# Kernel tuning notes

Measured on AMD Instinct MI355X. Metric: run time of the kernel, lower is better.

Reference implementation:

```python
import jax, jax.numpy as jnp
import numpy as np

N, E, D, H = 50000, 600000, 128, 128
SLOPE = 0.01  # default negative_slope of F.leaky_relu / nn.LeakyReLU


def leaky(x):
    return jnp.where(x >= 0, x, SLOPE * x)


def gcn_conv(x, src, dst, W, b, n):
    """PyG GCNConv: x' = D^{-1/2}(A+I)D^{-1/2} (x W) + b, symmetric norm with self-loops."""
    h = x @ W  # [n, out]
    ones = jnp.ones(src.shape[0], h.dtype)
    deg = jax.ops.segment_sum(ones, dst, num_segments=n) + 1.0  # +1 for self-loop
    dinv = jax.lax.rsqrt(deg)  # deg >= 1 always
    norm = dinv[src] * dinv[dst]  # per-edge coefficient
    msg = h[src] * norm[:, None]  # gather + scale: [E, out]
    agg = jax.ops.segment_sum(msg, dst, num_segments=n)  # scatter-add
    agg = agg + h * (dinv * dinv)[:, None]  # self-loop term
    return agg + b


def setup_inputs() -> dict:
    key = jax.random.key(0)
    ks = jax.random.split(key, 16)
    kaiming = lambda k, fi, fo: jax.random.normal(k, (fi, fo), jnp.float32) * np.sqrt(2.0 / fi)
    return {
        "x": jax.random.normal(ks[0], (N, D), jnp.float32),
        "edge_index": jax.random.randint(ks[1], (2, E), 0, N, jnp.int64 if jax.config.jax_enable_x64 else jnp.int32),
        "gen_data": jax.random.normal(ks[2], (N, H), jnp.float32),
        "Wc1": kaiming(ks[3], D, H), "bc1": jnp.zeros((H,), jnp.float32),
        "Wc2": kaiming(ks[4], H, H), "bc2": jnp.zeros((H,), jnp.float32),
        "Wm1": kaiming(ks[5], H, H), "bm1": jnp.zeros((H,), jnp.float32),
        "Wm2": kaiming(ks[6], H, H), "bm2": jnp.zeros((H,), jnp.float32),
        "Wp1": kaiming(ks[7], H, H), "bp1": jnp.zeros((H,), jnp.float32),
        "Wp2": kaiming(ks[8], H, H), "bp2": jnp.zeros((H,), jnp.float32),
    }


def reference(x, edge_index, gen_data, Wc1, bc1, Wc2, bc2, Wm1, bm1, Wm2, bm2, Wp1, bp1, Wp2, bp2):
    src, dst = edge_index[0], edge_index[1]
    lambd = 0.5
    # GraphEncoder4Link
    h = leaky(gcn_conv(x, src, dst, Wc1, bc1, N))
    h = leaky(gcn_conv(h, src, dst, Wc2, bc2, N) + h)
    h = leaky((leaky(h @ Wm1 + bm1) @ Wm2 + bm2) + h)
    # lambd interpolation with gen_data
    out = lambd * h + (1.0 - lambd) * gen_data
    # proj MLP
    out = leaky(leaky(out @ Wp1 + bp1) @ Wp2 + bp2)
    return out
```

## Files before the change

kernel.cpp:

```cpp
#include <hip/hip_runtime.h>
#include <cstdint>
#include <cstddef>

#define HH 128
#define SLOPE 0.01f

typedef __attribute__((ext_vector_type(8))) __bf16 bf16x8;
typedef __attribute__((ext_vector_type(8))) unsigned short ushort8v;
typedef __attribute__((ext_vector_type(4))) float f32x4;

__device__ __forceinline__ float lrelu(float x) { return x >= 0.f ? x : SLOPE * x; }
__device__ __forceinline__ unsigned short f2b(float f) {
  union { float f; unsigned u; } v; v.f = f;
  unsigned r = v.u + 0x7fffu + ((v.u >> 16) & 1u);
  return (unsigned short)(r >> 16);
}
__device__ __forceinline__ float b2f(unsigned short u) {
  union { unsigned u; float f; } v; v.u = ((unsigned)u) << 16; return v.f;
}

__device__ __forceinline__ int lofs(int r, int k) {
  return (r << 7) + ((((k >> 3) ^ r) & 15) << 3) + (k & 7);
}

#define WAVE_SYNC() asm volatile("s_waitcnt lgkmcnt(0)" ::: "memory")

__device__ __forceinline__ void gll16(const void* g, void* l) {
  __builtin_amdgcn_global_load_lds((const __attribute__((address_space(1))) void*)g,
                                   (__attribute__((address_space(3))) void*)l, 16, 0, 0);
}


__global__ __launch_bounds__(256) void count_kernel(const int* __restrict__ dst,
                                                    int* __restrict__ cnt,
                                                    int* __restrict__ rank, int nE) {
  int e = blockIdx.x * 256 + threadIdx.x;
  if (e < nE) rank[e] = atomicAdd(&cnt[dst[e]], 1);
}

__global__ __launch_bounds__(1024) void scan1_kernel(int* __restrict__ cnt,
                                                     int* __restrict__ rowptr,
                                                     int* __restrict__ bsum,
                                                     float* __restrict__ dinv, int n) {
  __shared__ int wsum[16];
  const int tid = threadIdx.x;
  const int lane = tid & 63, wid = tid >> 6;
  int i = blockIdx.x * 1024 + tid;
  int v = (i < n) ? cnt[i] : 0;
  int vp = (v + 7) & ~7;
  int x = vp;
#pragma unroll
  for (int off = 1; off < 64; off <<= 1) {
    int y = __shfl_up(x, off, 64);
    if (lane >= off) x += y;
  }
  if (lane == 63) wsum[wid] = x;
  __syncthreads();
  if (tid == 0) {
    int s = 0;
#pragma unroll
    for (int w = 0; w < 16; ++w) { int t = wsum[w]; wsum[w] = s; s += t; }
    bsum[blockIdx.x] = s;
  }
  __syncthreads();
  if (i < n) {
    rowptr[i] = wsum[wid] + x - vp;
    dinv[i] = rsqrtf((float)v + 1.0f);
  }
}

__global__ __launch_bounds__(64) void scan2_kernel(int* __restrict__ bsum, int nb,
                                                   int* __restrict__ rowptr, int n) {
  int lane = threadIdx.x;
  int v = (lane < nb) ? bsum[lane] : 0;
  int x = v;
#pragma unroll
  for (int off = 1; off < 64; off <<= 1) {
    int y = __shfl_up(x, off, 64);
    if (lane >= off) x += y;
  }
  int tot = __shfl(x, nb - 1);
  if (lane < nb) bsum[lane] = x - v;
  if (lane == 0) rowptr[n] = tot;
}

__global__ __launch_bounds__(1024) void scan3_kernel(int* __restrict__ rowptr,
                                                     const int* __restrict__ bsum, int n) {
  int i = blockIdx.x * 1024 + threadIdx.x;
  if (i < n) rowptr[i] += bsum[blockIdx.x];
}

__global__ __launch_bounds__(256) void fill_kernel(const int* __restrict__ src,
                                                   const int* __restrict__ dst,
                                                   const int* __restrict__ rowptr,
                                                   const int* __restrict__ rank,
                                                   const float* __restrict__ dinv,
                                                   int2* __restrict__ csr, int nE) {
  int e = blockIdx.x * 256 + threadIdx.x;
  if (e >= nE) return;
  int d = dst[e], s = src[e];
  int pos = rowptr[d] + rank[e];
  int2 ent;
  ent.x = s;
  ent.y = __float_as_int(dinv[s] * dinv[d]);
  csr[pos] = ent;
}

__global__ __launch_bounds__(256) void pack_kernel(const float* W0, const float* W1,
                                                   const float* W2, const float* W3,
                                                   const float* W4, const float* W5,
                                                   unsigned short* __restrict__ out) {
  const float* Ws[6] = {W0, W1, W2, W3, W4, W5};
  const float* W = Ws[blockIdx.y];
  int f = blockIdx.x * 256 + threadIdx.x;
  int j = f & 7, L = (f >> 3) & 63, c = (f >> 9) & 7, t = f >> 12;
  int k = t * 32 + (L >> 4) * 8 + j;
  int n = c * 16 + (L & 15);
  out[(size_t)blockIdx.y * 16384 + f] = f2b(W[k * HH + n]);
}


__device__ __forceinline__ void mfma_ldsW(const bf16x8 af[4],
                                          const unsigned short* __restrict__ Wl,
                                          int lane, f32x4 acc[8]) {
#pragma unroll
  for (int c = 0; c < 8; ++c) acc[c] = (f32x4){0.f, 0.f, 0.f, 0.f};
#pragma unroll
  for (int t = 0; t < 4; ++t) {
    bf16x8 wf[8];
#pragma unroll
    for (int c = 0; c < 8; ++c) wf[c] = *(const bf16x8*)&Wl[(t * 8 + c) * 512 + lane * 8];
#pragma unroll
    for (int c = 0; c < 8; ++c)
      acc[c] = __builtin_amdgcn_mfma_f32_16x16x32_bf16(af[t], wf[c], acc[c], 0, 0, 0);
  }
}

__device__ __forceinline__ void lds_afrags16(const unsigned short* __restrict__ Tl,
                                             int m, int quad, bf16x8 af[4]) {
#pragma unroll
  for (int t = 0; t < 4; ++t)
    af[t] = *(const bf16x8*)&Tl[lofs(m, t * 32 + quad * 8)];
}


__global__ __launch_bounds__(256, 1) void gemm_conv(const float* __restrict__ A,
                                                    const unsigned short* __restrict__ Wp,
                                                    unsigned short* __restrict__ out, int nrows) {
  __shared__ __align__(16) unsigned short Wl[16384];
  const int tid = threadIdx.x;
  const int lane = tid & 63, wave = tid >> 6;
  const int row0 = blockIdx.x * 64 + wave * 16;
  const int m = lane & 15, quad = lane >> 4;

#pragma unroll
  for (int i = 0; i < 8; ++i)
    gll16((const uint4*)Wp + i * 256 + tid, (uint4*)Wl + i * 256 + wave * 64);

  const int gr = row0 + m;
  const bool rok = gr < nrows;
  const float* Arow = A + (size_t)gr * HH;
  bf16x8 af[4];
#pragma unroll
  for (int t = 0; t < 4; ++t) {
    const int k = t * 32 + quad * 8;
    float4 lo = make_float4(0.f, 0.f, 0.f, 0.f), hi = lo;
    if (rok) {
      lo = *(const float4*)(Arow + k);
      hi = *(const float4*)(Arow + k + 4);
    }
    union { ushort8v u; bf16x8 b; } cv;
    cv.u[0] = f2b(lo.x); cv.u[1] = f2b(lo.y); cv.u[2] = f2b(lo.z); cv.u[3] = f2b(lo.w);
    cv.u[4] = f2b(hi.x); cv.u[5] = f2b(hi.y); cv.u[6] = f2b(hi.z); cv.u[7] = f2b(hi.w);
    af[t] = cv.b;
  }

  __syncthreads();

  f32x4 acc[8];
  mfma_ldsW(af, Wl, lane, acc);

#pragma unroll
  for (int c = 0; c < 8; ++c) {
    int col = c * 16 + m;
#pragma unroll
    for (int g = 0; g < 4; ++g) {
      int row = row0 + quad * 4 + g;
      if (row < nrows) out[(size_t)row * HH + col] = f2b(acc[c][g]);
    }
  }
}


template <int RES, int OUTBF>
__global__ __launch_bounds__(256) void agg_kernel(const unsigned short* __restrict__ h,
                                                  const int* __restrict__ rowptr,
                                                  const int2* __restrict__ csr,
                                                  const float* __restrict__ dinv,
                                                  const float* __restrict__ bias,
                                                  const float* __restrict__ res,
                                                  void* __restrict__ outv, int n) {
  int node = blockIdx.x * 4 + (threadIdx.x >> 6);
  if (node >= n) return;
  const int lane = threadIdx.x & 63;
  const int p = lane >> 5;
  const int c4 = (lane & 31) << 2;
  int j = rowptr[node];
  const int end = rowptr[node + 1];

  const float di = dinv[node];
  const ushort4 hs = *(const ushort4*)(h + (size_t)node * HH + c4);
  const float4 b = *(const float4*)(bias + c4);
  float4 rr = make_float4(0.f, 0.f, 0.f, 0.f);
  if (RES) rr = *(const float4*)(res + (size_t)node * HH + c4);

  float a0 = 0.f, a1 = 0.f, a2 = 0.f, a3 = 0.f;
  for (; j < end; j += 8) {
    int2 e[4];
    ushort4 r[4];
#pragma unroll
    for (int q = 0; q < 4; ++q) e[q] = csr[j + 2 * q + p];
#pragma unroll
    for (int q = 0; q < 4; ++q) r[q] = *(const ushort4*)(h + (size_t)e[q].x * HH + c4);
#pragma unroll
    for (int q = 0; q < 4; ++q) {
      float nv = __int_as_float(e[q].y);
      a0 = fmaf(b2f(r[q].x), nv, a0); a1 = fmaf(b2f(r[q].y), nv, a1);
      a2 = fmaf(b2f(r[q].z), nv, a2); a3 = fmaf(b2f(r[q].w), nv, a3);
    }
  }

  a0 += __shfl_xor(a0, 32);
  a1 += __shfl_xor(a1, 32);
  a2 += __shfl_xor(a2, 32);
  a3 += __shfl_xor(a3, 32);

  if (p == 0) {
    const float d2 = di * di;
    float o0 = a0 + b2f(hs.x) * d2 + b.x + rr.x;
    float o1 = a1 + b2f(hs.y) * d2 + b.y + rr.y;
    float o2 = a2 + b2f(hs.z) * d2 + b.z + rr.z;
    float o3 = a3 + b2f(hs.w) * d2 + b.w + rr.w;
    o0 = lrelu(o0); o1 = lrelu(o1); o2 = lrelu(o2); o3 = lrelu(o3);
    if (OUTBF) {
      ushort4 o;
      o.x = f2b(o0); o.y = f2b(o1); o.z = f2b(o2); o.w = f2b(o3);
      *(ushort4*)((unsigned short*)outv + (size_t)node * HH + c4) = o;
    } else {
      *(float4*)((float*)outv + (size_t)node * HH + c4) = make_float4(o0, o1, o2, o3);
    }
  }
}


__global__ __launch_bounds__(256, 1) void fusedMLP(const unsigned short* __restrict__ f2bf,
                                                   const unsigned short* __restrict__ Wm1p,
                                                   const unsigned short* __restrict__ Wm2p,
                                                   const unsigned short* __restrict__ Wp1p,
                                                   const unsigned short* __restrict__ Wp2p,
                                                   const float* __restrict__ bm1,
                                                   const float* __restrict__ bm2,
                                                   const float* __restrict__ bp1,
                                                   const float* __restrict__ bp2,
                                                   const float* __restrict__ gen,
                                                   float* __restrict__ out, int n) {
  __shared__ __align__(16) unsigned short Wl[2][16384];
  __shared__ __align__(16) unsigned short Tl[4][16 * HH];
  const int tid = threadIdx.x;
  const int lane = tid & 63, wave = tid >> 6;
  const int row0 = blockIdx.x * 64 + wave * 16;
  const int m = lane & 15, quad = lane >> 4;
  unsigned short* T = Tl[wave];

#pragma unroll
  for (int i = 0; i < 8; ++i) {
    gll16((const uint4*)Wm1p + i * 256 + tid, (uint4*)Wl[0] + i * 256 + wave * 64);
    gll16((const uint4*)Wm2p + i * 256 + tid, (uint4*)Wl[1] + i * 256 + wave * 64);
  }

#pragma unroll
  for (int i = 0; i < 4; ++i) {
    int idx = i * 64 + lane;
    int r = idx >> 4, k = (idx & 15) << 3;
    int gr = row0 + r;
    ushort8v v = {0, 0, 0, 0, 0, 0, 0, 0};
    if (gr < n) v = *(const ushort8v*)(f2bf + (size_t)gr * HH + k);
    *(ushort8v*)&T[lofs(r, k)] = v;
  }

  ushort4 genb[8];
#pragma unroll
  for (int i = 0; i < 8; ++i) {
    int idx = i * 64 + lane;
    int r = idx >> 5, c4 = (idx & 31) << 2;
    int gr = row0 + r;
    float4 v = make_float4(0.f, 0.f, 0.f, 0.f);
    if (gr < n) v = *(const float4*)(gen + (size_t)gr * HH + c4);
    genb[i].x = f2b(v.x); genb[i].y = f2b(v.y); genb[i].z = f2b(v.z); genb[i].w = f2b(v.w);
  }

  float bvAll[4][8];
#pragma unroll
  for (int cc = 0; cc < 8; ++cc) {
    int col = cc * 16 + m;
    bvAll[0][cc] = bm1[col];
    bvAll[1][cc] = bm2[col];
    bvAll[2][cc] = bp1[col];
    bvAll[3][cc] = bp2[col];
  }

  __syncthreads();

  bf16x8 af[4];
  f32x4 acc[8];

  lds_afrags16(T, m, quad, af);
  unsigned f2res[8][2];
#pragma unroll
  for (int cc = 0; cc < 8; ++cc) {
    int col = cc * 16 + m;
#pragma unroll
    for (int gp = 0; gp < 2; ++gp) {
      int lr = quad * 4 + gp * 2;
      f2res[cc][gp] = (unsigned)T[lofs(lr, col)] | ((unsigned)T[lofs(lr + 1, col)] << 16);
    }
  }
  mfma_ldsW(af, Wl[0], lane, acc);
  WAVE_SYNC();
#pragma unroll
  for (int cc = 0; cc < 8; ++cc) {
    int col = cc * 16 + m;
#pragma unroll
    for (int g = 0; g < 4; ++g)
      T[lofs(quad * 4 + g, col)] = f2b(lrelu(acc[cc][g] + bvAll[0][cc]));
  }
  __syncthreads();

#pragma unroll
  for (int i = 0; i < 8; ++i)
    gll16((const uint4*)Wp1p + i * 256 + tid, (uint4*)Wl[0] + i * 256 + wave * 64);

  lds_afrags16(T, m, quad, af);
  WAVE_SYNC();
#pragma unroll
  for (int i = 0; i < 8; ++i) {
    int idx = i * 64 + lane;
    int r = idx >> 5, c4 = (idx & 31) << 2;
    *(ushort4*)&T[lofs(r, c4)] = genb[i];
  }
  mfma_ldsW(af, Wl[1], lane, acc);
  WAVE_SYNC();
#pragma unroll
  for (int cc = 0; cc < 8; ++cc) {
    int col = cc * 16 + m;
#pragma unroll
    for (int g = 0; g < 4; ++g) {
      int lr = quad * 4 + g;
      unsigned fr = f2res[cc][g >> 1];
      float f2v = b2f((unsigned short)((g & 1) ? (fr >> 16) : (fr & 0xffffu)));
      float v = lrelu(acc[cc][g] + bvAll[1][cc] + f2v);
      float gv = b2f(T[lofs(lr, col)]);
      T[lofs(lr, col)] = f2b(0.5f * (v + gv));
    }
  }
  __syncthreads();

#pragma unroll
  for (int i = 0; i < 8; ++i)
    gll16((const uint4*)Wp2p + i * 256 + tid, (uint4*)Wl[1] + i * 256 + wave * 64);

  lds_afrags16(T, m, quad, af);
  mfma_ldsW(af, Wl[0], lane, acc);
  WAVE_SYNC();
#pragma unroll
  for (int cc = 0; cc < 8; ++cc) {
    int col = cc * 16 + m;
#pragma unroll
    for (int g = 0; g < 4; ++g)
      T[lofs(quad * 4 + g, col)] = f2b(lrelu(acc[cc][g] + bvAll[2][cc]));
  }
  __syncthreads();

  lds_afrags16(T, m, quad, af);
  mfma_ldsW(af, Wl[1], lane, acc);
#pragma unroll
  for (int cc = 0; cc < 8; ++cc) {
    int col = cc * 16 + m;
#pragma unroll
    for (int g = 0; g < 4; ++g) {
      int row = row0 + quad * 4 + g;
      if (row < n) out[(size_t)row * HH + col] = lrelu(acc[cc][g] + bvAll[3][cc]);
    }
  }
}


extern "C" void kernel_launch(void* const* d_in, const int* in_sizes, int n_in,
                              void* d_out, int out_size, void* d_ws, size_t ws_size,
                              hipStream_t stream) {
  const float* x   = (const float*)d_in[0];
  const int* ei    = (const int*)d_in[1];
  const float* gen = (const float*)d_in[2];
  const float* Wc1 = (const float*)d_in[3];
  const float* bc1 = (const float*)d_in[4];
  const float* Wc2 = (const float*)d_in[5];
  const float* bc2 = (const float*)d_in[6];
  const float* Wm1 = (const float*)d_in[7];
  const float* bm1 = (const float*)d_in[8];
  const float* Wm2 = (const float*)d_in[9];
  const float* bm2 = (const float*)d_in[10];
  const float* Wp1 = (const float*)d_in[11];
  const float* bp1 = (const float*)d_in[12];
  const float* Wp2 = (const float*)d_in[13];
  const float* bp2 = (const float*)d_in[14];

  const int N = in_sizes[0] / HH;
  const int E = in_sizes[1] / 2;
  const int* src = ei;
  const int* dst = ei + E;

  const size_t Epad = (size_t)E + 8 * (size_t)N;

  char* ws = (char*)d_ws;
  size_t off = 0;
  auto alloc = [&](size_t bytes) { void* p = ws + off; off += (bytes + 255) & ~(size_t)255; return p; };
  float* dinv            = (float*)alloc((size_t)N * 4);
  int*   rowptr          = (int*)  alloc((size_t)(N + 1) * 4);
  int*   cnt             = (int*)  alloc((size_t)N * 4);
  int*   bsum            = (int*)  alloc((size_t)64 * 4);
  int*   rank            = (int*)  alloc((size_t)E * 4);
  int2*  csr             = (int2*) alloc(Epad * 8);
  unsigned short* h_bf   = (unsigned short*)alloc((size_t)N * HH * 2);
  unsigned short* t2_bf  = (unsigned short*)alloc((size_t)N * HH * 2);
  unsigned short* f2_bf  = (unsigned short*)alloc((size_t)N * HH * 2);
  float* f1_f32          = (float*)alloc((size_t)N * HH * 4);
  unsigned short* packed = (unsigned short*)alloc((size_t)6 * 16384 * 2);
  float* fOut = (float*)d_out;

  const int cblocks = (N + 63) / 64;
  const int eblocks = (E + 255) / 256;
  const int ablocks = (N + 3) / 4;
  const int sblocks = (N + 1023) / 1024;

  pack_kernel<<<dim3(64, 6), 256, 0, stream>>>(Wc1, Wc2, Wm1, Wm2, Wp1, Wp2, packed);

  hipMemsetAsync(cnt, 0, (size_t)N * 4, stream);
  hipMemsetAsync(csr, 0, Epad * 8, stream);
  count_kernel<<<eblocks, 256, 0, stream>>>(dst, cnt, rank, E);
  scan1_kernel<<<sblocks, 1024, 0, stream>>>(cnt, rowptr, bsum, dinv, N);
  scan2_kernel<<<1, 64, 0, stream>>>(bsum, sblocks, rowptr, N);
  scan3_kernel<<<sblocks, 1024, 0, stream>>>(rowptr, bsum, N);
  fill_kernel<<<eblocks, 256, 0, stream>>>(src, dst, rowptr, rank, dinv, csr, E);

  gemm_conv<<<cblocks, 256, 0, stream>>>(x, packed + 0 * 16384, h_bf, N);
  agg_kernel<0, 0><<<ablocks, 256, 0, stream>>>(h_bf, rowptr, csr, dinv, bc1, nullptr, f1_f32, N);
  gemm_conv<<<cblocks, 256, 0, stream>>>(f1_f32, packed + 1 * 16384, t2_bf, N);
  agg_kernel<1, 1><<<ablocks, 256, 0, stream>>>(t2_bf, rowptr, csr, dinv, bc2, f1_f32, f2_bf, N);
  fusedMLP<<<cblocks, 256, 0, stream>>>(f2_bf,
                                        packed + 2 * 16384, packed + 3 * 16384,
                                        packed + 4 * 16384, packed + 5 * 16384,
                                        bm1, bm2, bp1, bp2, gen, fOut, N);
}
```

Before: 280.8 us.

## Merge preprocessing launches: pack+count, scan2 into scan3, fill into first GEMM

Combines the weight pack and edge-count kernels into one launch, folds the single-block scan of block sums into each scan3 block, and runs CSR fill blocks alongside the first GEMM in one grid. The two memsets become one by making cnt and csr contiguous in the workspace. This cuts kernel launches and the serial gaps between small kernels. The trade-offs are redundant per-block scan work and fill blocks that now run under the GEMM's launch bounds and LDS allocation.

```diff
diff --git a/kernel.cpp b/kernel.cpp
--- a/kernel.cpp
+++ b/kernel.cpp
@@ -31,12 +31,30 @@
 }
 
 
-__global__ __launch_bounds__(256) void count_kernel(const int* __restrict__ dst,
+__global__ __launch_bounds__(256) void k_pack_count(const float* W0, const float* W1,
+                                                    const float* W2, const float* W3,
+                                                    const float* W4, const float* W5,
+                                                    unsigned short* __restrict__ outp,
+                                                    const int* __restrict__ dst,
                                                     int* __restrict__ cnt,
                                                     int* __restrict__ rank, int nE) {
-  int e = blockIdx.x * 256 + threadIdx.x;
-  if (e < nE) rank[e] = atomicAdd(&cnt[dst[e]], 1);
-}
+  const int bb = blockIdx.x;
+  const int tid = threadIdx.x;
+  if (bb < 384) {
+    const float* Ws[6] = {W0, W1, W2, W3, W4, W5};
+    const int mat = bb >> 6;
+    const float* W = Ws[mat];
+    int f = (bb & 63) * 256 + tid;
+    int j = f & 7, L = (f >> 3) & 63, c = (f >> 9) & 7, t = f >> 12;
+    int k = t * 32 + (L >> 4) * 8 + j;
+    int n = c * 16 + (L & 15);
+    outp[(size_t)mat * 16384 + f] = f2b(W[k * HH + n]);
+  } else {
+    int e = (bb - 384) * 256 + tid;
+    if (e < nE) rank[e] = atomicAdd(&cnt[dst[e]], 1);
+  }
+}
+
 
 __global__ __launch_bounds__(1024) void scan1_kernel(int* __restrict__ cnt,
                                                      int* __restrict__ rowptr,
@@ -69,54 +87,26 @@
   }
 }
 
-__global__ __launch_bounds__(64) void scan2_kernel(int* __restrict__ bsum, int nb,
-                                                   int* __restrict__ rowptr, int n) {
-  int lane = threadIdx.x;
-  int v = (lane < nb) ? bsum[lane] : 0;
-  int x = v;
-#pragma unroll
-  for (int off = 1; off < 64; off <<= 1) {
-    int y = __shfl_up(x, off, 64);
-    if (lane >= off) x += y;
-  }
-  int tot = __shfl(x, nb - 1);
-  if (lane < nb) bsum[lane] = x - v;
-  if (lane == 0) rowptr[n] = tot;
-}
-
 __global__ __launch_bounds__(1024) void scan3_kernel(int* __restrict__ rowptr,
-                                                     const int* __restrict__ bsum, int n) {
-  int i = blockIdx.x * 1024 + threadIdx.x;
-  if (i < n) rowptr[i] += bsum[blockIdx.x];
-}
-
-__global__ __launch_bounds__(256) void fill_kernel(const int* __restrict__ src,
-                                                   const int* __restrict__ dst,
-                                                   const int* __restrict__ rowptr,
-                                                   const int* __restrict__ rank,
-                                                   const float* __restrict__ dinv,
-                                                   int2* __restrict__ csr, int nE) {
-  int e = blockIdx.x * 256 + threadIdx.x;
-  if (e >= nE) return;
-  int d = dst[e], s = src[e];
-  int pos = rowptr[d] + rank[e];
-  int2 ent;
-  ent.x = s;
-  ent.y = __float_as_int(dinv[s] * dinv[d]);
-  csr[pos] = ent;
-}
-
-__global__ __launch_bounds__(256) void pack_kernel(const float* W0, const float* W1,
-                                                   const float* W2, const float* W3,
-                                                   const float* W4, const float* W5,
-                                                   unsigned short* __restrict__ out) {
-  const float* Ws[6] = {W0, W1, W2, W3, W4, W5};
-  const float* W = Ws[blockIdx.y];
-  int f = blockIdx.x * 256 + threadIdx.x;
-  int j = f & 7, L = (f >> 3) & 63, c = (f >> 9) & 7, t = f >> 12;
-  int k = t * 32 + (L >> 4) * 8 + j;
-  int n = c * 16 + (L & 15);
-  out[(size_t)blockIdx.y * 16384 + f] = f2b(W[k * HH + n]);
+                                                     const int* __restrict__ bsum,
+                                                     int n, int nb) {
+  __shared__ int spfx, stot;
+  const int tid = threadIdx.x;
+  if (tid < 64) {
+    int v = (tid < nb) ? bsum[tid] : 0;
+    int x = v;
+#pragma unroll
+    for (int off = 1; off < 64; off <<= 1) {
+      int y = __shfl_up(x, off, 64);
+      if (tid >= off) x += y;
+    }
+    if (tid == (int)blockIdx.x) spfx = x - v;
+    if (tid == nb - 1) stot = x;
+  }
+  __syncthreads();
+  int i = blockIdx.x * 1024 + tid;
+  if (i < n) rowptr[i] += spfx;
+  if (blockIdx.x == 0 && tid == 0) rowptr[n] = stot;
 }
 
 
@@ -143,14 +133,14 @@
     af[t] = *(const bf16x8*)&Tl[lofs(m, t * 32 + quad * 8)];
 }
 
-
-__global__ __launch_bounds__(256, 1) void gemm_conv(const float* __restrict__ A,
-                                                    const unsigned short* __restrict__ Wp,
-                                                    unsigned short* __restrict__ out, int nrows) {
-  __shared__ __align__(16) unsigned short Wl[16384];
+__device__ __forceinline__ void gemm_body(unsigned short* Wl,
+                                          const float* __restrict__ A,
+                                          const unsigned short* __restrict__ Wp,
+                                          unsigned short* __restrict__ out,
+                                          int nrows, int vb) {
   const int tid = threadIdx.x;
   const int lane = tid & 63, wave = tid >> 6;
-  const int row0 = blockIdx.x * 64 + wave * 16;
+  const int row0 = vb * 64 + wave * 16;
   const int m = lane & 15, quad = lane >> 4;
 
 #pragma unroll
@@ -189,6 +179,40 @@
       if (row < nrows) out[(size_t)row * HH + col] = f2b(acc[c][g]);
     }
   }
+}
+
+
+__global__ __launch_bounds__(256, 1) void k_gemm_fill(const float* __restrict__ A,
+                                                      const unsigned short* __restrict__ Wp,
+                                                      unsigned short* __restrict__ out, int nrows,
+                                                      int gemmBlocks,
+                                                      const int* __restrict__ src,
+                                                      const int* __restrict__ dst,
+                                                      const int* __restrict__ rowptr,
+                                                      const int* __restrict__ rank,
+                                                      const float* __restrict__ dinv,
+                                                      int2* __restrict__ csr, int nE) {
+  __shared__ __align__(16) unsigned short Wl[16384];
+  const int bb = blockIdx.x;
+  if (bb < gemmBlocks) {
+    gemm_body(Wl, A, Wp, out, nrows, bb);
+  } else {
+    int e = (bb - gemmBlocks) * 256 + threadIdx.x;
+    if (e >= nE) return;
+    int d = dst[e], s = src[e];
+    int pos = rowptr[d] + rank[e];
+    int2 ent;
+    ent.x = s;
+    ent.y = __float_as_int(dinv[s] * dinv[d]);
+    csr[pos] = ent;
+  }
+}
+
+__global__ __launch_bounds__(256, 1) void gemm_conv(const float* __restrict__ A,
+                                                    const unsigned short* __restrict__ Wp,
+                                                    unsigned short* __restrict__ out, int nrows) {
+  __shared__ __align__(16) unsigned short Wl[16384];
+  gemm_body(Wl, A, Wp, out, nrows, blockIdx.x);
 }
 
 
@@ -426,9 +450,9 @@
   auto alloc = [&](size_t bytes) { void* p = ws + off; off += (bytes + 255) & ~(size_t)255; return p; };
   float* dinv            = (float*)alloc((size_t)N * 4);
   int*   rowptr          = (int*)  alloc((size_t)(N + 1) * 4);
-  int*   cnt             = (int*)  alloc((size_t)N * 4);
   int*   bsum            = (int*)  alloc((size_t)64 * 4);
   int*   rank            = (int*)  alloc((size_t)E * 4);
+  int*   cnt             = (int*)  alloc((size_t)N * 4);
   int2*  csr             = (int2*) alloc(Epad * 8);
   unsigned short* h_bf   = (unsigned short*)alloc((size_t)N * HH * 2);
   unsigned short* t2_bf  = (unsigned short*)alloc((size_t)N * HH * 2);
@@ -442,17 +466,19 @@
   const int ablocks = (N + 3) / 4;
   const int sblocks = (N + 1023) / 1024;
 
-  pack_kernel<<<dim3(64, 6), 256, 0, stream>>>(Wc1, Wc2, Wm1, Wm2, Wp1, Wp2, packed);
-
-  hipMemsetAsync(cnt, 0, (size_t)N * 4, stream);
-  hipMemsetAsync(csr, 0, Epad * 8, stream);
-  count_kernel<<<eblocks, 256, 0, stream>>>(dst, cnt, rank, E);
+  size_t zbytes = (size_t)((char*)csr + Epad * 8 - (char*)cnt);
+  hipMemsetAsync(cnt, 0, zbytes, stream);
+
+  k_pack_count<<<384 + eblocks, 256, 0, stream>>>(Wc1, Wc2, Wm1, Wm2, Wp1, Wp2, packed,
+                                                  dst, cnt, rank, E);
+
   scan1_kernel<<<sblocks, 1024, 0, stream>>>(cnt, rowptr, bsum, dinv, N);
-  scan2_kernel<<<1, 64, 0, stream>>>(bsum, sblocks, rowptr, N);
-  scan3_kernel<<<sblocks, 1024, 0, stream>>>(rowptr, bsum, N);
-  fill_kernel<<<eblocks, 256, 0, stream>>>(src, dst, rowptr, rank, dinv, csr, E);
-
-  gemm_conv<<<cblocks, 256, 0, stream>>>(x, packed + 0 * 16384, h_bf, N);
+  scan3_kernel<<<sblocks, 1024, 0, stream>>>(rowptr, bsum, N, sblocks);
+
+  k_gemm_fill<<<cblocks + eblocks, 256, 0, stream>>>(x, packed + 0 * 16384, h_bf, N,
+                                                     cblocks, src, dst, rowptr, rank,
+                                                     dinv, csr, E);
+
   agg_kernel<0, 0><<<ablocks, 256, 0, stream>>>(h_bf, rowptr, csr, dinv, bc1, nullptr, f1_f32, N);
   gemm_conv<<<cblocks, 256, 0, stream>>>(f1_f32, packed + 1 * 16384, t2_bf, N);
   agg_kernel<1, 1><<<ablocks, 256, 0, stream>>>(t2_bf, rowptr, csr, dinv, bc2, f1_f32, f2_bf, N);
```

Measured after the change: 263.2 us. -6.3%, faster.
